# Performance work log

Measured on AMD Instinct MI355X. Metric: run time of the kernel, lower is better.

Reference implementation:

```python
import jax, jax.numpy as jnp
import numpy as np

LN_EPS = 1e-5

def _lstm_scan(xp, w_hh):
    # xp: [T, B, 4H] precomputed input projections (+bias); w_hh: [4H, H]
    H = w_hh.shape[1]
    B = xp.shape[1]
    def step(carry, x_t):
        h, c = carry
        gates = x_t + h @ w_hh.T
        i, f, g, o = jnp.split(gates, 4, axis=-1)  # torch gate order i,f,g,o
        i = jax.nn.sigmoid(i); f = jax.nn.sigmoid(f)
        g = jnp.tanh(g); o = jax.nn.sigmoid(o)
        c = f * c + i * g
        h = o * jnp.tanh(c)
        return (h, c), h
    init = (jnp.zeros((B, H), xp.dtype), jnp.zeros((B, H), xp.dtype))
    _, hs = jax.lax.scan(step, init, xp)
    return hs  # [T, B, H]

def setup_inputs() -> dict:
    key = jax.random.key(0)
    ks = jax.random.split(key, 16)
    B, T, V, E, K = 64, 512, 21128, 256, 9
    H4 = 4 * E
    s = 0.08  # small init scale for numerical stability
    return {
        'word_ids': jax.random.randint(ks[0], (B, T), 0, V, dtype=jnp.int32),
        'label_ids': jax.random.randint(ks[1], (B, T), 0, K, dtype=jnp.int32),
        'embed_table': jax.random.normal(ks[2], (V, E), jnp.float32) * s,
        'w_ih_f': jax.random.normal(ks[3], (H4, E), jnp.float32) * s,
        'w_hh_f': jax.random.normal(ks[4], (H4, E), jnp.float32) * s,
        'b_f': jnp.zeros((H4,), jnp.float32),
        'w_ih_b': jax.random.normal(ks[5], (H4, E), jnp.float32) * s,
        'w_hh_b': jax.random.normal(ks[6], (H4, E), jnp.float32) * s,
        'b_b': jnp.zeros((H4,), jnp.float32),
        'ln_gamma': jnp.ones((2 * E,), jnp.float32),
        'ln_beta': jnp.zeros((2 * E,), jnp.float32),
        'cls_w': jax.random.normal(ks[7], (K, 2 * E), jnp.float32) * s,
        'cls_b': jnp.zeros((K,), jnp.float32),
        'crf_start': jax.random.normal(ks[8], (K,), jnp.float32) * 0.1,
        'crf_end': jax.random.normal(ks[9], (K,), jnp.float32) * 0.1,
        'crf_trans': jax.random.normal(ks[10], (K, K), jnp.float32) * 0.1,
    }

def reference(word_ids, label_ids, embed_table, w_ih_f, w_hh_f, b_f,
              w_ih_b, w_hh_b, b_b, ln_gamma, ln_beta, cls_w, cls_b,
              crf_start, crf_end, crf_trans):
    # Embedding (dropout is identity at eval)
    emb = embed_table[word_ids]                      # [B, T, E]

    # BiLSTM: precompute input projections once, scan over time
    xf = (emb @ w_ih_f.T + b_f).transpose(1, 0, 2)   # [T, B, 4H]
    hf = _lstm_scan(xf, w_hh_f)                      # [T, B, H]
    xb = (emb[:, ::-1] @ w_ih_b.T + b_b).transpose(1, 0, 2)
    hb = _lstm_scan(xb, w_hh_b)[::-1]                # reverse back to forward time
    seq = jnp.concatenate([hf, hb], axis=-1).transpose(1, 0, 2)  # [B, T, 2H]

    # LayerNorm over last dim
    mu = seq.mean(-1, keepdims=True)
    var = ((seq - mu) ** 2).mean(-1, keepdims=True)
    seq = (seq - mu) * jax.lax.rsqrt(var + LN_EPS) * ln_gamma + ln_beta

    logits = seq @ cls_w.T + cls_b                   # [B, T, K] = CRF emissions

    # --- CRF log-likelihood (no mask: all positions valid) ---
    tags = label_ids
    # numerator: score of gold path
    em_score = jnp.take_along_axis(logits, tags[..., None], axis=-1)[..., 0]  # [B, T]
    trans_score = crf_trans[tags[:, :-1], tags[:, 1:]].sum(axis=1)            # [B]
    numerator = (crf_start[tags[:, 0]] + em_score.sum(axis=1)
                 + trans_score + crf_end[tags[:, -1]])                        # [B]

    # denominator: forward algorithm (logsumexp DP over time)
    alpha0 = crf_start[None, :] + logits[:, 0]       # [B, K]
    em_rest = logits[:, 1:].transpose(1, 0, 2)       # [T-1, B, K]
    def step(alpha, em_t):
        # alpha: [B, K] (prev tag), crf_trans: [K, K], em_t: [B, K] (next tag)
        new = jax.scipy.special.logsumexp(
            alpha[:, :, None] + crf_trans[None, :, :] + em_t[:, None, :], axis=1)
        return new, None
    alpha, _ = jax.lax.scan(step, alpha0, em_rest)
    logZ = jax.scipy.special.logsumexp(alpha + crf_end[None, :], axis=1)      # [B]

    llh = (numerator - logZ).sum()   # torchcrf default reduction='sum'
    loss = -llh
    preds = jnp.argmax(logits, axis=-1)
    return (loss, preds)
```

## Files before the change

kernel.cpp:

```cpp
#include <hip/hip_runtime.h>
#include <cstdint>
#include <cmath>

typedef __attribute__((ext_vector_type(8))) short short8;
typedef __attribute__((ext_vector_type(4))) float floatx4;

__device__ __forceinline__ unsigned pk_bf16(float x, float y) {
    unsigned ux = __float_as_uint(x); ux = ux + 0x7fffu + ((ux >> 16) & 1u);
    unsigned uy = __float_as_uint(y); uy = uy + 0x7fffu + ((uy >> 16) & 1u);
    return (ux >> 16) | (uy & 0xffff0000u);
}
__device__ __forceinline__ unsigned short bf16r(float x) {
    unsigned ux = __float_as_uint(x);
    return (unsigned short)((ux + 0x7fffu + ((ux >> 16) & 1u)) >> 16);
}
__device__ __forceinline__ float bf16d(unsigned short v) {
    return __uint_as_float((unsigned)v << 16);
}

__global__ __launch_bounds__(256) void proj_kernel(
    const int* __restrict__ word_ids, const float* __restrict__ embed,
    const float* __restrict__ w_ih_f, const float* __restrict__ b_f,
    const float* __restrict__ w_ih_b, const float* __restrict__ b_b,
    unsigned short* __restrict__ XF, unsigned short* __restrict__ XB,
    int t0, int lgL)
{
    __shared__ unsigned short As[64][264];
    __shared__ unsigned short Bs[64][264];
    __shared__ int idx[64];

    const int tid = threadIdx.x;
    const int nt  = blockIdx.x;
    const int dir = blockIdx.y;
    const int Lm1 = (1 << lgL) - 1;
    const float* __restrict__ W    = dir ? w_ih_b : w_ih_f;
    const float* __restrict__ bias = dir ? b_b : b_f;
    unsigned short* __restrict__ Xout = dir ? XB : XF;

    if (tid < 64) {
        int n  = nt * 64 + tid;
        int b  = n >> lgL;
        int tl = n & Lm1;
        int tg = dir ? (511 - (t0 + tl)) : (t0 + tl);
        idx[tid] = word_ids[b * 512 + tg];
    }
    __syncthreads();

    #pragma unroll
    for (int i = 0; i < 16; ++i) {
        int flat = i * 256 + tid;
        int r  = flat >> 6;
        int kq = flat & 63;
        floatx4 a = *(const floatx4*)&embed[(size_t)idx[r] * 256 + kq * 4];
        *(uint2*)&As[r][kq * 4] = make_uint2(pk_bf16(a.x, a.y), pk_bf16(a.z, a.w));
    }
    __syncthreads();

    const int w    = tid >> 6;
    const int lane = tid & 63;
    const int q    = lane >> 4;
    const int lr   = lane & 15;

    short8 af[8];
    #pragma unroll
    for (int ks = 0; ks < 8; ++ks)
        af[ks] = *(const short8*)&As[w * 16 + lr][ks * 32 + q * 8];

    int bb[4], tt4[4];
    #pragma unroll
    for (int reg = 0; reg < 4; ++reg) {
        int n  = nt * 64 + w * 16 + q * 4 + reg;
        bb[reg]  = n >> lgL;
        tt4[reg] = n & Lm1;
    }

    for (int jt = 0; jt < 16; ++jt) {
        __syncthreads();
        #pragma unroll
        for (int i = 0; i < 16; ++i) {
            int flat = i * 256 + tid;
            int r  = flat >> 6;
            int kq = flat & 63;
            floatx4 wv = *(const floatx4*)&W[(size_t)(jt * 64 + r) * 256 + kq * 4];
            *(uint2*)&Bs[r][kq * 4] = make_uint2(pk_bf16(wv.x, wv.y), pk_bf16(wv.z, wv.w));
        }
        __syncthreads();

        #pragma unroll
        for (int jt4 = 0; jt4 < 4; ++jt4) {
            floatx4 c = {0.f, 0.f, 0.f, 0.f};
            #pragma unroll
            for (int ks = 0; ks < 8; ++ks) {
                short8 bf = *(const short8*)&Bs[jt4 * 16 + lr][ks * 32 + q * 8];
                c = __builtin_amdgcn_mfma_f32_16x16x32_bf16(af[ks], bf, c, 0, 0, 0);
            }
            int j = jt * 64 + jt4 * 16 + lr;
            float bj = bias[j];
            #pragma unroll
            for (int reg = 0; reg < 4; ++reg)
                Xout[((size_t)tt4[reg] * 64 + bb[reg]) * 1024 + j] = bf16r(c[reg] + bj);
        }
    }
}

__global__ __launch_bounds__(512, 1)
__attribute__((amdgpu_num_vgpr(256)))
void lstm_scan(
    const unsigned short* __restrict__ XF, const unsigned short* __restrict__ XB,
    const float* __restrict__ w_hh_f, const float* __restrict__ w_hh_b,
    float* __restrict__ hf, float* __restrict__ hb,
    float* __restrict__ state_c, float* __restrict__ state_h, int t0, int t1)
{
    __shared__ unsigned short Ah[2][264];
    __shared__ float scr[4][2][256];
    __shared__ short8 Wlds[8 * 2 * 8 * 64];

    const int blk = blockIdx.x;
    const int dir = blk >> 5;
    const int grp = blk & 31;
    const int B0  = grp * 2;
    const unsigned short* __restrict__ X = dir ? XB : XF;
    const float* __restrict__ Whh = dir ? w_hh_b : w_hh_f;
    float* __restrict__ Hout      = dir ? hb : hf;

    const int tid  = threadIdx.x;
    const int w    = tid >> 6;
    const int lane = tid & 63;
    const int q    = lane >> 4;
    const int lr   = lane & 15;
    const int g    = w >> 1;
    const int uh   = w & 1;

    short8 wreg[6][8];
    #pragma unroll
    for (int ntl = 0; ntl < 8; ++ntl) {
        const float* wrow = &Whh[(size_t)(g * 256 + uh * 128 + ntl * 16 + lr) * 256];
        #pragma unroll
        for (int ks = 0; ks < 8; ++ks) {
            floatx4 a = *(const floatx4*)&wrow[ks * 32 + q * 8];
            floatx4 b = *(const floatx4*)&wrow[ks * 32 + q * 8 + 4];
            union { uint4 u4; short8 s; } cv;
            cv.u4 = make_uint4(pk_bf16(a.x, a.y), pk_bf16(a.z, a.w),
                               pk_bf16(b.x, b.y), pk_bf16(b.z, b.w));
            if (ntl < 6) wreg[ntl][ks] = cv.s;
            else         Wlds[((w * 2 + (ntl - 6)) * 8 + ks) * 64 + lane] = cv.s;
        }
    }

    const int b_p = tid >> 8;
    const int u_p = tid & 255;
    const int sgi = (dir * 64 + B0 + b_p) * 256 + u_p;
    float cst = 0.f;
    float hlast = 0.f;
    if (t0 == 0) {
        Ah[b_p][u_p] = 0;
    } else {
        cst = state_c[sgi];
        hlast = state_h[sgi];
        Ah[b_p][u_p] = bf16r(hlast);
    }

    for (int t = t0; t < t1; ++t) {
        float xg[4];
        {
            const unsigned short* Xc = &X[((size_t)(t - t0) * 64 + B0 + b_p) * 1024 + u_p];
            #pragma unroll
            for (int gg = 0; gg < 4; ++gg)
                xg[gg] = bf16d(Xc[gg * 256]);
        }
        __syncthreads();

        short8 af[8];
        #pragma unroll
        for (int ks = 0; ks < 8; ++ks)
            af[ks] = *(const short8*)&Ah[lr & 1][ks * 32 + q * 8];
        #pragma unroll
        for (int ntl = 0; ntl < 8; ++ntl) {
            floatx4 c = {0.f, 0.f, 0.f, 0.f};
            #pragma unroll
            for (int ks = 0; ks < 8; ++ks) {
                if (ntl < 6)
                    c = __builtin_amdgcn_mfma_f32_16x16x32_bf16(af[ks], wreg[ntl][ks], c, 0, 0, 0);
                else
                    c = __builtin_amdgcn_mfma_f32_16x16x32_bf16(
                            af[ks], Wlds[((w * 2 + (ntl - 6)) * 8 + ks) * 64 + lane], c, 0, 0, 0);
            }
            if (q == 0) {
                scr[g][0][uh * 128 + ntl * 16 + lr] = c[0];
                scr[g][1][uh * 128 + ntl * 16 + lr] = c[1];
            }
        }
        __syncthreads();

        {
            float gi = scr[0][b_p][u_p] + xg[0];
            float gf = scr[1][b_p][u_p] + xg[1];
            float gg = scr[2][b_p][u_p] + xg[2];
            float go = scr[3][b_p][u_p] + xg[3];
            float ig = 1.f / (1.f + expf(-gi));
            float fg = 1.f / (1.f + expf(-gf));
            float gv = tanhf(gg);
            float og = 1.f / (1.f + expf(-go));
            cst = fg * cst + ig * gv;
            float h = og * tanhf(cst);
            hlast = h;
            int tt = dir ? (511 - t) : t;
            Hout[((size_t)tt * 64 + B0 + b_p) * 256 + u_p] = h;
            Ah[b_p][u_p] = bf16r(h);
        }
    }

    state_c[sgi] = cst;
    state_h[sgi] = hlast;
}

__global__ __launch_bounds__(256) void ln_cls_kernel(
    const float* __restrict__ hf, const float* __restrict__ hb,
    const float* __restrict__ gamma, const float* __restrict__ beta,
    const float* __restrict__ cls_w, const float* __restrict__ cls_b,
    float* __restrict__ logits, float* __restrict__ dout)
{
    const int lane = threadIdx.x & 63;
    const int wid  = threadIdx.x >> 6;
    const int pos  = blockIdx.x * 4 + wid;
    const int b = pos >> 9;
    const int t = pos & 511;

    float4 v0 = *(const float4*)&hf[((size_t)t * 64 + b) * 256 + lane * 4];
    float4 v1 = *(const float4*)&hb[((size_t)t * 64 + b) * 256 + lane * 4];
    float x[8] = {v0.x, v0.y, v0.z, v0.w, v1.x, v1.y, v1.z, v1.w};

    float s = 0.f;
    #pragma unroll
    for (int i = 0; i < 8; ++i) s += x[i];
    #pragma unroll
    for (int off = 32; off > 0; off >>= 1) s += __shfl_xor(s, off, 64);
    float mu = s * (1.f / 512.f);

    float d[8];
    float sq = 0.f;
    #pragma unroll
    for (int i = 0; i < 8; ++i) { d[i] = x[i] - mu; sq += d[i] * d[i]; }
    #pragma unroll
    for (int off = 32; off > 0; off >>= 1) sq += __shfl_xor(sq, off, 64);
    float rs = 1.f / sqrtf(sq * (1.f / 512.f) + 1e-5f);

    float4 g0  = *(const float4*)&gamma[lane * 4];
    float4 g1  = *(const float4*)&gamma[256 + lane * 4];
    float4 be0 = *(const float4*)&beta[lane * 4];
    float4 be1 = *(const float4*)&beta[256 + lane * 4];
    float y[8];
    y[0] = d[0] * rs * g0.x + be0.x; y[1] = d[1] * rs * g0.y + be0.y;
    y[2] = d[2] * rs * g0.z + be0.z; y[3] = d[3] * rs * g0.w + be0.w;
    y[4] = d[4] * rs * g1.x + be1.x; y[5] = d[5] * rs * g1.y + be1.y;
    y[6] = d[6] * rs * g1.z + be1.z; y[7] = d[7] * rs * g1.w + be1.w;

    float lgt[9];
    #pragma unroll
    for (int c = 0; c < 9; ++c) {
        float4 w0 = *(const float4*)&cls_w[c * 512 + lane * 4];
        float4 w1 = *(const float4*)&cls_w[c * 512 + 256 + lane * 4];
        float p = y[0] * w0.x + y[1] * w0.y + y[2] * w0.z + y[3] * w0.w
                + y[4] * w1.x + y[5] * w1.y + y[6] * w1.z + y[7] * w1.w;
        #pragma unroll
        for (int off = 32; off > 0; off >>= 1) p += __shfl_xor(p, off, 64);
        lgt[c] = p + cls_b[c];
    }
    if (lane == 0) {
        int bestc = 0;
        float bestv = lgt[0];
        #pragma unroll
        for (int c = 1; c < 9; ++c)
            if (lgt[c] > bestv) { bestv = lgt[c]; bestc = c; }
        dout[1 + pos] = (float)bestc;
        #pragma unroll
        for (int c = 0; c < 9; ++c) logits[(size_t)pos * 9 + c] = lgt[c];
    }
}

__global__ __launch_bounds__(64) void crf_kernel(
    const float* __restrict__ logits, const int* __restrict__ label_ids,
    const float* __restrict__ crf_start, const float* __restrict__ crf_end,
    const float* __restrict__ crf_trans, float* __restrict__ llh)
{
    __shared__ float Ts[9][12];
    const int b = blockIdx.x;
    const int lane = threadIdx.x;
    if (lane < 81) Ts[lane / 9][lane % 9] = crf_trans[lane];
    __syncthreads();

    const float* __restrict__ em  = &logits[(size_t)b * 512 * 9];
    const int* __restrict__ tags  = &label_ids[b * 512];

    float part = 0.f;
    for (int t = lane; t < 512; t += 64) {
        int tg = tags[t];
        part += em[t * 9 + tg];
        if (t < 511) part += Ts[tg][tags[t + 1]];
    }
    #pragma unroll
    for (int off = 32; off > 0; off >>= 1) part += __shfl_xor(part, off, 64);
    float numer = part + crf_start[tags[0]] + crf_end[tags[511]];

    const int j = (lane < 9) ? lane : 0;
    float alpha = crf_start[j] + em[j];
    for (int t = 1; t < 512; ++t) {
        float av[9];
        float m = -1e30f;
        #pragma unroll
        for (int i = 0; i < 9; ++i) {
            float ai = __shfl(alpha, i, 64);
            av[i] = ai + Ts[i][j];
            m = fmaxf(m, av[i]);
        }
        float ssum = 0.f;
        #pragma unroll
        for (int i = 0; i < 9; ++i) ssum += expf(av[i] - m);
        alpha = m + logf(ssum) + em[t * 9 + j];
    }
    float v = (lane < 9) ? (alpha + crf_end[j]) : -1e30f;
    float mm = v;
    #pragma unroll
    for (int off = 32; off > 0; off >>= 1) mm = fmaxf(mm, __shfl_xor(mm, off, 64));
    float es = (lane < 9) ? expf(v - mm) : 0.f;
    #pragma unroll
    for (int off = 32; off > 0; off >>= 1) es += __shfl_xor(es, off, 64);
    if (lane == 0) llh[b] = numer - (mm + logf(es));
}

__global__ __launch_bounds__(64) void final_reduce(
    const float* __restrict__ llh, float* __restrict__ dout)
{
    float v = llh[threadIdx.x];
    #pragma unroll
    for (int off = 32; off > 0; off >>= 1) v += __shfl_xor(v, off, 64);
    if (threadIdx.x == 0) dout[0] = -v;
}

extern "C" void kernel_launch(void* const* d_in, const int* in_sizes, int n_in,
                              void* d_out, int out_size, void* d_ws, size_t ws_size,
                              hipStream_t stream)
{
    const int*   word_ids  = (const int*)d_in[0];
    const int*   label_ids = (const int*)d_in[1];
    const float* embed     = (const float*)d_in[2];
    const float* w_ih_f    = (const float*)d_in[3];
    const float* w_hh_f    = (const float*)d_in[4];
    const float* b_f       = (const float*)d_in[5];
    const float* w_ih_b    = (const float*)d_in[6];
    const float* w_hh_b    = (const float*)d_in[7];
    const float* b_b       = (const float*)d_in[8];
    const float* ln_gamma  = (const float*)d_in[9];
    const float* ln_beta   = (const float*)d_in[10];
    const float* cls_w     = (const float*)d_in[11];
    const float* cls_b     = (const float*)d_in[12];
    const float* crf_start = (const float*)d_in[13];
    const float* crf_end   = (const float*)d_in[14];
    const float* crf_trans = (const float*)d_in[15];

    char* w = (char*)d_ws;
    auto alloc = [&](size_t bytes) -> char* {
        char* p = w; w += (bytes + 255) & ~(size_t)255; return p;
    };
    float* hf      = (float*)alloc((size_t)8388608 * 4);
    float* hb      = (float*)alloc((size_t)8388608 * 4);
    float* logits  = (float*)alloc((size_t)294912 * 4);
    float* state_c = (float*)alloc((size_t)32768 * 4);
    float* state_h = (float*)alloc((size_t)32768 * 4);
    float* llh     = (float*)alloc((size_t)64 * 4);
    size_t fixed   = (size_t)(w - (char*)d_ws);

    int L = 512;
    while (L > 32 && fixed + (size_t)L * 262144 > ws_size) L >>= 1;
    unsigned short* XF = (unsigned short*)alloc((size_t)L * 65536 * 2);
    unsigned short* XB = (unsigned short*)alloc((size_t)L * 65536 * 2);
    int lgL = 31 - __builtin_clz((unsigned)L);

    for (int t0 = 0; t0 < 512; t0 += L) {
        proj_kernel<<<dim3(L, 2), 256, 0, stream>>>(
            word_ids, embed, w_ih_f, b_f, w_ih_b, b_b, XF, XB, t0, lgL);
        lstm_scan<<<64, 512, 0, stream>>>(
            XF, XB, w_hh_f, w_hh_b, hf, hb, state_c, state_h, t0, t0 + L);
    }
    ln_cls_kernel<<<8192, 256, 0, stream>>>(
        hf, hb, ln_gamma, ln_beta, cls_w, cls_b, logits, (float*)d_out);
    crf_kernel<<<64, 64, 0, stream>>>(
        logits, label_ids, crf_start, crf_end, crf_trans, llh);
    final_reduce<<<1, 64, 0, stream>>>(llh, (float*)d_out);
}
```

Baseline: 1.476 ms.

## Remap LSTM gate columns per wave to drop scratch exchange and one barrier

Reassigns the recurrent-weight tiles so each wave owns all four gates for the same 32 hidden units. The gate nonlinearities can then be computed directly from the MFMA accumulators in registers, with no LDS scratch round-trip. The hidden-state buffer is double-buffered, which removes one of the two per-step barriers, and the next step's input projections are prefetched into registers. The cost is that only a quarter of the lanes (q==0) do the elementwise work, and register pressure rises.

```diff
diff --git a/kernel.cpp b/kernel.cpp
--- a/kernel.cpp
+++ b/kernel.cpp
@@ -16,6 +16,13 @@
 }
 __device__ __forceinline__ float bf16d(unsigned short v) {
     return __uint_as_float((unsigned)v << 16);
+}
+
+__device__ __forceinline__ void bar_lds() {
+    __builtin_amdgcn_sched_barrier(0);
+    asm volatile("s_waitcnt lgkmcnt(0)" ::: "memory");
+    __builtin_amdgcn_s_barrier();
+    __builtin_amdgcn_sched_barrier(0);
 }
 
 __global__ __launch_bounds__(256) void proj_kernel(
@@ -111,8 +118,7 @@
     float* __restrict__ hf, float* __restrict__ hb,
     float* __restrict__ state_c, float* __restrict__ state_h, int t0, int t1)
 {
-    __shared__ unsigned short Ah[2][264];
-    __shared__ float scr[4][2][256];
+    __shared__ unsigned short Ah[2][2][264];
     __shared__ short8 Wlds[8 * 2 * 8 * 64];
 
     const int blk = blockIdx.x;
@@ -128,13 +134,13 @@
     const int lane = tid & 63;
     const int q    = lane >> 4;
     const int lr   = lane & 15;
-    const int g    = w >> 1;
-    const int uh   = w & 1;
+    const int u0   = w * 32 + lr;
 
     short8 wreg[6][8];
     #pragma unroll
-    for (int ntl = 0; ntl < 8; ++ntl) {
-        const float* wrow = &Whh[(size_t)(g * 256 + uh * 128 + ntl * 16 + lr) * 256];
+    for (int nt = 0; nt < 8; ++nt) {
+        const int gt = nt >> 1, ut = nt & 1;
+        const float* wrow = &Whh[(size_t)(gt * 256 + w * 32 + ut * 16 + lr) * 256];
         #pragma unroll
         for (int ks = 0; ks < 8; ++ks) {
             floatx4 a = *(const floatx4*)&wrow[ks * 32 + q * 8];
@@ -142,76 +148,106 @@
             union { uint4 u4; short8 s; } cv;
             cv.u4 = make_uint4(pk_bf16(a.x, a.y), pk_bf16(a.z, a.w),
                                pk_bf16(b.x, b.y), pk_bf16(b.z, b.w));
-            if (ntl < 6) wreg[ntl][ks] = cv.s;
-            else         Wlds[((w * 2 + (ntl - 6)) * 8 + ks) * 64 + lane] = cv.s;
-        }
-    }
-
-    const int b_p = tid >> 8;
-    const int u_p = tid & 255;
-    const int sgi = (dir * 64 + B0 + b_p) * 256 + u_p;
-    float cst = 0.f;
-    float hlast = 0.f;
-    if (t0 == 0) {
-        Ah[b_p][u_p] = 0;
-    } else {
-        cst = state_c[sgi];
-        hlast = state_h[sgi];
-        Ah[b_p][u_p] = bf16r(hlast);
-    }
+            if (nt < 6) wreg[nt][ks] = cv.s;
+            else        Wlds[((w * 2 + (nt - 6)) * 8 + ks) * 64 + lane] = cv.s;
+        }
+    }
+
+    float cst[2][2] = {{0.f, 0.f}, {0.f, 0.f}};
+    float hl [2][2] = {{0.f, 0.f}, {0.f, 0.f}};
+    float xg [4][2][2];
+
+    if (q == 0) {
+        if (t0 != 0) {
+            #pragma unroll
+            for (int b = 0; b < 2; ++b)
+                #pragma unroll
+                for (int ut = 0; ut < 2; ++ut) {
+                    int sgi = (dir * 64 + B0 + b) * 256 + u0 + ut * 16;
+                    cst[b][ut] = state_c[sgi];
+                    hl [b][ut] = state_h[sgi];
+                }
+        }
+        #pragma unroll
+        for (int b = 0; b < 2; ++b)
+            #pragma unroll
+            for (int ut = 0; ut < 2; ++ut)
+                Ah[t0 & 1][b][u0 + ut * 16] = bf16r(hl[b][ut]);
+        #pragma unroll
+        for (int gg = 0; gg < 4; ++gg)
+            #pragma unroll
+            for (int b = 0; b < 2; ++b)
+                #pragma unroll
+                for (int ut = 0; ut < 2; ++ut)
+                    xg[gg][b][ut] = bf16d(
+                        X[((size_t)(B0 + b)) * 1024 + gg * 256 + u0 + ut * 16]);
+    }
+    bar_lds();
+
+    const floatx4 zero = {0.f, 0.f, 0.f, 0.f};
 
     for (int t = t0; t < t1; ++t) {
-        float xg[4];
-        {
-            const unsigned short* Xc = &X[((size_t)(t - t0) * 64 + B0 + b_p) * 1024 + u_p];
+        const int p = t & 1;
+
+        floatx4 c[4][2];
+        #pragma unroll
+        for (int gt = 0; gt < 4; ++gt) { c[gt][0] = zero; c[gt][1] = zero; }
+        #pragma unroll
+        for (int ks = 0; ks < 8; ++ks) {
+            short8 af = *(const short8*)&Ah[p][lr & 1][ks * 32 + q * 8];
+            #pragma unroll
+            for (int nt = 0; nt < 8; ++nt) {
+                const int gt = nt >> 1, ut = nt & 1;
+                short8 bf = (nt < 6) ? wreg[nt][ks]
+                                     : Wlds[((w * 2 + (nt - 6)) * 8 + ks) * 64 + lane];
+                c[gt][ut] = __builtin_amdgcn_mfma_f32_16x16x32_bf16(af, bf, c[gt][ut], 0, 0, 0);
+            }
+        }
+
+        if (q == 0) {
+            #pragma unroll
+            for (int b = 0; b < 2; ++b)
+                #pragma unroll
+                for (int ut = 0; ut < 2; ++ut) {
+                    float gi = c[0][ut][b] + xg[0][b][ut];
+                    float gf = c[1][ut][b] + xg[1][b][ut];
+                    float gv = c[2][ut][b] + xg[2][b][ut];
+                    float go = c[3][ut][b] + xg[3][b][ut];
+                    float ig = 1.f / (1.f + expf(-gi));
+                    float fg = 1.f / (1.f + expf(-gf));
+                    float gc = tanhf(gv);
+                    float og = 1.f / (1.f + expf(-go));
+                    float cs = fg * cst[b][ut] + ig * gc;
+                    cst[b][ut] = cs;
+                    float h = og * tanhf(cs);
+                    hl[b][ut] = h;
+                    Ah[p ^ 1][b][u0 + ut * 16] = bf16r(h);
+                    int tt = dir ? (511 - t) : t;
+                    Hout[((size_t)tt * 64 + B0 + b) * 256 + u0 + ut * 16] = h;
+                }
+            int tn = (t + 1 < t1) ? (t + 1 - t0) : 0;
             #pragma unroll
             for (int gg = 0; gg < 4; ++gg)
-                xg[gg] = bf16d(Xc[gg * 256]);
-        }
-        __syncthreads();
-
-        short8 af[8];
-        #pragma unroll
-        for (int ks = 0; ks < 8; ++ks)
-            af[ks] = *(const short8*)&Ah[lr & 1][ks * 32 + q * 8];
-        #pragma unroll
-        for (int ntl = 0; ntl < 8; ++ntl) {
-            floatx4 c = {0.f, 0.f, 0.f, 0.f};
-            #pragma unroll
-            for (int ks = 0; ks < 8; ++ks) {
-                if (ntl < 6)
-                    c = __builtin_amdgcn_mfma_f32_16x16x32_bf16(af[ks], wreg[ntl][ks], c, 0, 0, 0);
-                else
-                    c = __builtin_amdgcn_mfma_f32_16x16x32_bf16(
-                            af[ks], Wlds[((w * 2 + (ntl - 6)) * 8 + ks) * 64 + lane], c, 0, 0, 0);
+                #pragma unroll
+                for (int b = 0; b < 2; ++b)
+                    #pragma unroll
+                    for (int ut = 0; ut < 2; ++ut)
+                        xg[gg][b][ut] = bf16d(
+                            X[((size_t)tn * 64 + B0 + b) * 1024 + gg * 256 + u0 + ut * 16]);
+        }
+        bar_lds();
+    }
+
+    if (q == 0) {
+        #pragma unroll
+        for (int b = 0; b < 2; ++b)
+            #pragma unroll
+            for (int ut = 0; ut < 2; ++ut) {
+                int sgi = (dir * 64 + B0 + b) * 256 + u0 + ut * 16;
+                state_c[sgi] = cst[b][ut];
+                state_h[sgi] = hl[b][ut];
             }
-            if (q == 0) {
-                scr[g][0][uh * 128 + ntl * 16 + lr] = c[0];
-                scr[g][1][uh * 128 + ntl * 16 + lr] = c[1];
-            }
-        }
-        __syncthreads();
-
-        {
-            float gi = scr[0][b_p][u_p] + xg[0];
-            float gf = scr[1][b_p][u_p] + xg[1];
-            float gg = scr[2][b_p][u_p] + xg[2];
-            float go = scr[3][b_p][u_p] + xg[3];
-            float ig = 1.f / (1.f + expf(-gi));
-            float fg = 1.f / (1.f + expf(-gf));
-            float gv = tanhf(gg);
-            float og = 1.f / (1.f + expf(-go));
-            cst = fg * cst + ig * gv;
-            float h = og * tanhf(cst);
-            hlast = h;
-            int tt = dir ? (511 - t) : t;
-            Hout[((size_t)tt * 64 + B0 + b_p) * 256 + u_p] = h;
-            Ah[b_p][u_p] = bf16r(h);
-        }
-    }
-
-    state_c[sgi] = cst;
-    state_h[sgi] = hlast;
+    }
 }
 
 __global__ __launch_bounds__(256) void ln_cls_kernel(
```

New measurement: 2.312 ms. 56.7% more time.
